# Kernel tuning notes

Hardware: AMD Instinct MI355X
Metric: run time of the kernel (lower is better)

The kernel has to match this reference:

```python
import jax, jax.numpy as jnp
import numpy as np

N = 50000   # number of cells/nodes
C = 256     # in_channels
H = 4       # num_heads
D = 64      # out_channels (per-head)
E = 800000  # number of edges (avg degree 16)


def setup_inputs() -> dict:
    key = jax.random.key(0)
    ks = jax.random.split(key, 10)
    s = 1.0 / np.sqrt(C)  # torch nn.Linear default init bound
    u = lambda k, shape: jax.random.uniform(k, shape, jnp.float32, -s, s)
    return {
        "query_input": jax.random.normal(ks[0], (N, C), jnp.float32),
        "source_input": jax.random.normal(ks[1], (N, C), jnp.float32),
        "Wq_w": u(ks[2], (H * D, C)), "Wq_b": u(ks[3], (H * D,)),
        "Wk_w": u(ks[4], (H * D, C)), "Wk_b": u(ks[5], (H * D,)),
        "Wv_w": u(ks[6], (H * D, C)), "Wv_b": u(ks[7], (H * D,)),
        "edge_index": jax.random.randint(ks[8], (2, E), 0, N),
        "edge_weight": jax.random.uniform(ks[9], (E,), jnp.float32),
    }


def reference(query_input, source_input, Wq_w, Wq_b, Wk_w, Wk_b, Wv_w, Wv_b,
              edge_index, edge_weight):
    n = query_input.shape[0]
    q = (query_input @ Wq_w.T + Wq_b).reshape(n, H, D)
    k = (source_input @ Wk_w.T + Wk_b).reshape(n, H, D)
    v = (source_input @ Wv_w.T + Wv_b).reshape(n, H, D)

    # --- linear (kernelized) attention, global Frobenius normalization ---
    qs = q / jnp.linalg.norm(q)
    ksn = k / jnp.linalg.norm(k)
    kvs = jnp.einsum('lhm,lhd->hmd', ksn, v)               # [H,M,D]
    attn_num = jnp.einsum('nhm,hmd->nhd', qs, kvs)
    attn_num = attn_num + v.sum(axis=0)[None]              # + vs_sum broadcast
    ks_sum = ksn.sum(axis=0)                               # [H,M]
    normalizer = jnp.einsum('nhm,hm->nh', qs, ks_sum)[..., None] + jnp.float32(n)
    attn_out = attn_num / normalizer                       # [N,H,D]

    # --- GCN aggregation on value: out[col] += w * d_norm_in * d_norm_out * v[row] ---
    row, col = edge_index[0], edge_index[1]
    d = jnp.zeros((n,), jnp.float32).at[col].add(1.0)      # in-degree on col
    d_norm_in = jnp.sqrt(1.0 / d[col])
    d_norm_out = jnp.sqrt(1.0 / d[row])
    val = jnp.nan_to_num(edge_weight * d_norm_in * d_norm_out,
                         nan=0.0, posinf=0.0, neginf=0.0)  # [E]
    gathered = v[row] * val[:, None, None]                 # [E,H,D]
    gcn_out = jax.ops.segment_sum(gathered, col, num_segments=n)  # [N,H,D]

    return (attn_out + gcn_out).mean(axis=1)               # [N,D]
```

## Files before the change

kernel.cpp:

```cpp
#include <hip/hip_runtime.h>
#include <hip/hip_bf16.h>

#define N_NODES 50000
#define N_EDGES 800000
#define NBUK 512
#define BWID 98
#define BCAP 2048
#define PCHUNK 1024
#define PBLK 782
#define NVS 32

typedef __bf16 bf16x8 __attribute__((ext_vector_type(8)));
typedef float f32x4 __attribute__((ext_vector_type(4)));

__device__ __forceinline__ unsigned short f2bf(float f) {
    unsigned int u = __builtin_bit_cast(unsigned int, f);
    u += 0x7fffu + ((u >> 16) & 1u);
    return (unsigned short)(u >> 16);
}
__device__ __forceinline__ float bf2f(unsigned short s) {
    return __uint_as_float((unsigned int)s << 16);
}

__device__ __forceinline__ void gld_lds16(const void* g, void* lds) {
    __builtin_amdgcn_global_load_lds(
        (const __attribute__((address_space(1))) unsigned int*)g,
        (__attribute__((address_space(3))) unsigned int*)lds, 16, 0, 0);
}

__global__ __launch_bounds__(256) void k_wprep(const float* __restrict__ Wv,
                                               const float* __restrict__ bv,
                                               unsigned short* __restrict__ wvbar,
                                               float* __restrict__ bvbar) {
    int idx = blockIdx.x * 256 + threadIdx.x;
    int d = idx >> 6;
    int c0 = (idx & 63) * 4;
    const float4* W4 = (const float4*)Wv;
    float4 w0 = W4[((d) * 256 + c0) >> 2];
    float4 w1 = W4[((64 + d) * 256 + c0) >> 2];
    float4 w2 = W4[((128 + d) * 256 + c0) >> 2];
    float4 w3 = W4[((192 + d) * 256 + c0) >> 2];
    ushort4 s;
    s.x = f2bf(0.25f * (w0.x + w1.x + w2.x + w3.x));
    s.y = f2bf(0.25f * (w0.y + w1.y + w2.y + w3.y));
    s.z = f2bf(0.25f * (w0.z + w1.z + w2.z + w3.z));
    s.w = f2bf(0.25f * (w0.w + w1.w + w2.w + w3.w));
    int ks = c0 >> 5;
    int q  = (c0 >> 3) & 3;
    int j0 = c0 & 7;
    int nf = d >> 4;
    int ln = d & 15;
    int base = ((ks * 4 + nf) * 64 + q * 16 + ln) * 8 + j0;
    *(ushort4*)&wvbar[base] = s;
    if (blockIdx.x == 0 && threadIdx.x < 64) {
        int t = threadIdx.x;
        bvbar[t] = 0.25f * (bv[t] + bv[64 + t] + bv[128 + t] + bv[192 + t]);
    }
}

__global__ __launch_bounds__(256) void k_part(const int* __restrict__ ei,
                                              const float* __restrict__ ew,
                                              int* __restrict__ gcur,
                                              uint2* __restrict__ bkt)
{
    __shared__ int hist[NBUK];
    __shared__ int cur[NBUK];
    const int t = threadIdx.x;
    const int e0 = blockIdx.x * PCHUNK;
    hist[t] = 0; hist[t + 256] = 0;
    __syncthreads();
    #pragma unroll
    for (int k = 0; k < PCHUNK / 256; ++k) {
        int e = e0 + k * 256 + t;
        if (e < N_EDGES) {
            int c = ei[N_EDGES + e];
            atomicAdd(&hist[c / BWID], 1);
        }
    }
    __syncthreads();
    {
        int b = t;
        if (hist[b]) cur[b] = b * BCAP + atomicAdd(&gcur[b], hist[b]);
        b = t + 256;
        if (hist[b]) cur[b] = b * BCAP + atomicAdd(&gcur[b], hist[b]);
    }
    __syncthreads();
    #pragma unroll
    for (int k = 0; k < PCHUNK / 256; ++k) {
        int e = e0 + k * 256 + t;
        if (e < N_EDGES) {
            int c = ei[N_EDGES + e];
            int b = c / BWID;
            int row = ei[e];
            float w = ew[e];
            int slot = atomicAdd(&cur[b], 1);
            if (slot < (b + 1) * BCAP) {
                uint2 en;
                en.x = ((unsigned int)row << 16) | (unsigned int)f2bf(w);
                en.y = (unsigned int)(c - b * BWID);
                bkt[slot] = en;
            }
        }
    }
}

__global__ __launch_bounds__(256) void k_bucket(const int* __restrict__ gcur,
                                                const uint2* __restrict__ bkt,
                                                int* __restrict__ deg,
                                                int* __restrict__ off,
                                                unsigned int* __restrict__ srt)
{
    __shared__ int hist[128];
    __shared__ int lcur[128];
    const int t = threadIdx.x;
    const int b = blockIdx.x;
    if (t < 128) hist[t] = 0;
    __syncthreads();
    const int cnt = min(gcur[b], BCAP);
    const uint2* base = bkt + (size_t)b * BCAP;
    for (int i = t; i < cnt; i += 256)
        atomicAdd(&hist[base[i].y], 1);
    __syncthreads();
    const int v = (t < 128) ? hist[t] : 0;
    #pragma unroll
    for (int d = 1; d < 128; d <<= 1) {
        int u = (t >= d && t < 128) ? hist[t - d] : 0;
        __syncthreads();
        if (t >= d && t < 128) hist[t] += u;
        __syncthreads();
    }
    if (t < 128) {
        int excl = hist[t] - v;
        lcur[t] = excl;
        if (t < BWID) {
            int col = b * BWID + t;
            if (col < N_NODES) {
                deg[col] = v;
                off[col] = b * BCAP + excl;
            }
        }
    }
    __syncthreads();
    unsigned int* sb = srt + (size_t)b * BCAP;
    for (int i = t; i < cnt; i += 256) {
        uint2 en = base[i];
        int pos = atomicAdd(&lcur[en.y], 1);
        sb[pos] = en.x;
    }
}

__global__ __launch_bounds__(256) void k_vbar(
    const float* __restrict__ Xs, const unsigned short* __restrict__ wvbar,
    const float* __restrict__ bvbar, const int* __restrict__ deg,
    unsigned short* __restrict__ vbarh, float* __restrict__ vsumr)
{
    __shared__ float lX[64 * 128];
    const int t = threadIdx.x;
    const int w = t >> 6;
    const int l = t & 63;
    const int ln = l & 15;
    const int q = l >> 4;
    const int n0 = blockIdx.x * 64;

    const char* Xc = (const char*)Xs;
    const bf16x8* Wf = (const bf16x8*)wvbar;
    const unsigned int swzl = ((unsigned int)(ln & 7)) << 4;
    const char* lrow = (const char*)&lX[(w * 16 + ln) * 128];

    f32x4 acc[4];
    #pragma unroll
    for (int nf = 0; nf < 4; ++nf) acc[nf] = (f32x4){0.f, 0.f, 0.f, 0.f};

    #pragma unroll
    for (int h = 0; h < 2; ++h) {
        #pragma unroll
        for (int i = 0; i < 8; ++i) {
            int r = w * 16 + i * 2 + (l >> 5);
            int g = n0 + r;
            int gc = (g < N_NODES) ? g : 0;
            unsigned int off = ((unsigned int)((l & 31) * 16))
                             ^ (((unsigned int)(r & 7)) << 4);
            const void* src = Xc + (size_t)gc * 1024 + (unsigned int)(h * 512) + off;
            gld_lds16(src, &lX[(w * 16 + i * 2) * 128]);
        }
        asm volatile("s_waitcnt vmcnt(0)" ::: "memory");
        __builtin_amdgcn_sched_barrier(0);

        #pragma unroll
        for (int ks2 = 0; ks2 < 4; ++ks2) {
            unsigned int c0 = (unsigned int)(ks2 * 128 + q * 32);
            float4 xa = *(const float4*)(lrow + (c0 ^ swzl));
            float4 xb = *(const float4*)(lrow + ((c0 + 16u) ^ swzl));
            bf16x8 A;
            A[0] = (__bf16)xa.x; A[1] = (__bf16)xa.y;
            A[2] = (__bf16)xa.z; A[3] = (__bf16)xa.w;
            A[4] = (__bf16)xb.x; A[5] = (__bf16)xb.y;
            A[6] = (__bf16)xb.z; A[7] = (__bf16)xb.w;
            int ks = h * 4 + ks2;
            #pragma unroll
            for (int nf = 0; nf < 4; ++nf) {
                bf16x8 b = Wf[(ks * 4 + nf) * 64 + l];
                acc[nf] = __builtin_amdgcn_mfma_f32_16x16x32_bf16(A, b, acc[nf], 0, 0, 0);
            }
        }
        if (h == 0) {
            asm volatile("s_waitcnt lgkmcnt(0)" ::: "memory");
            __builtin_amdgcn_sched_barrier(0);
        }
    }

    float bvb[4];
    #pragma unroll
    for (int nf = 0; nf < 4; ++nf) bvb[nf] = bvbar[nf * 16 + ln];
    float psum[4] = {0.f, 0.f, 0.f, 0.f};
    #pragma unroll
    for (int r4 = 0; r4 < 4; ++r4) {
        int g = n0 + w * 16 + q * 4 + r4;
        bool ok = g < N_NODES;
        float sc = 0.f;
        if (ok) {
            float dg = (float)deg[g];
            sc = (dg > 0.f) ? __frsqrt_rn(dg) : 0.f;
        }
        #pragma unroll
        for (int nf = 0; nf < 4; ++nf) {
            if (ok) {
                vbarh[g * 64 + nf * 16 + ln] = f2bf((acc[nf][r4] + bvb[nf]) * sc);
                psum[nf] += acc[nf][r4];
            }
        }
    }
    #pragma unroll
    for (int nf = 0; nf < 4; ++nf) {
        float v = psum[nf];
        v += __shfl_xor(v, 16, 64);
        v += __shfl_xor(v, 32, 64);
        psum[nf] = v;
    }
    if (l < 16) {
        int rep = (blockIdx.x * 4 + w) & (NVS - 1);
        #pragma unroll
        for (int nf = 0; nf < 4; ++nf)
            atomicAdd(&vsumr[rep * 64 + nf * 16 + ln], psum[nf]);
    }
}

__global__ __launch_bounds__(256) void k_gather(
    const int* __restrict__ off, const int* __restrict__ deg,
    const unsigned int* __restrict__ srt, const unsigned short* __restrict__ vbarh,
    const float* __restrict__ vsumr, const float* __restrict__ bvbar,
    float* __restrict__ out)
{
    const int t = threadIdx.x;
    const int lane = t & 63;
    const int n = blockIdx.x * 4 + (t >> 6);
    if (n >= N_NODES) return;
    const int e0 = off[n];
    const int dc = deg[n];
    const int e1 = e0 + dc;
    float acc = 0.f;
    int e = e0;
    for (; e + 3 < e1; e += 4) {
        unsigned int p0 = srt[e];
        unsigned int p1 = srt[e + 1];
        unsigned int p2 = srt[e + 2];
        unsigned int p3 = srt[e + 3];
        float a0 = __uint_as_float(p0 << 16) * bf2f(vbarh[(p0 >> 16) * 64 + lane]);
        float a1 = __uint_as_float(p1 << 16) * bf2f(vbarh[(p1 >> 16) * 64 + lane]);
        float a2 = __uint_as_float(p2 << 16) * bf2f(vbarh[(p2 >> 16) * 64 + lane]);
        float a3 = __uint_as_float(p3 << 16) * bf2f(vbarh[(p3 >> 16) * 64 + lane]);
        acc += (a0 + a1) + (a2 + a3);
    }
    for (; e < e1; ++e) {
        unsigned int p = srt[e];
        acc += __uint_as_float(p << 16) * bf2f(vbarh[(p >> 16) * 64 + lane]);
    }
    float dcf = (float)dc;
    float scn = (dcf > 0.f) ? __frsqrt_rn(dcf) : 0.f;
    float vs = 0.f;
    #pragma unroll
    for (int i = 0; i < NVS; ++i) vs += vsumr[i * 64 + lane];
    float aconst = vs * (1.0f / (float)N_NODES) + bvbar[lane];
    out[n * 64 + lane] = acc * scn + aconst;
}

extern "C" void kernel_launch(void* const* d_in, const int* in_sizes, int n_in,
                              void* d_out, int out_size, void* d_ws, size_t ws_size,
                              hipStream_t stream)
{
    const float* Xs = (const float*)d_in[1];
    const float* Wv = (const float*)d_in[6];
    const float* bv = (const float*)d_in[7];
    const int*   ei = (const int*)d_in[8];
    const float* ew = (const float*)d_in[9];
    float* out = (float*)d_out;

    unsigned short* vbarh = (unsigned short*)d_ws;
    uint2* bkt  = (uint2*)(vbarh + (size_t)N_NODES * 64);
    unsigned int* srt = (unsigned int*)(bkt + (size_t)NBUK * BCAP);
    unsigned short* wvbar = (unsigned short*)(srt + (size_t)NBUK * BCAP);
    float* bvbar   = (float*)(wvbar + 16384);
    float* vsumr   = bvbar + 64;
    int*   gcur    = (int*)(vsumr + NVS * 64);
    int*   deg     = gcur + NBUK;
    int*   off     = deg + N_NODES;

    hipMemsetAsync(vsumr, 0, (size_t)(NVS * 64 + NBUK) * 4, stream);
    k_wprep<<<16, 256, 0, stream>>>(Wv, bv, wvbar, bvbar);
    k_part<<<PBLK, 256, 0, stream>>>(ei, ew, gcur, bkt);
    k_bucket<<<NBUK, 256, 0, stream>>>(gcur, bkt, deg, off, srt);
    k_vbar<<<(N_NODES + 63) / 64, 256, 0, stream>>>(Xs, wvbar, bvbar, deg, vbarh, vsumr);
    k_gather<<<(NBUK * BWID) / 4, 256, 0, stream>>>(off, deg, srt, vbarh, vsumr, bvbar, out);
}
```

Before: 215.2 us.

## Stage edge partition and bucket sort through LDS for coalesced global writes

The partition kernel now processes larger chunks per block, does a local prefix sum over bucket counts, and sorts entries by bucket in shared memory before writing them out, so global stores to each bucket become contiguous runs instead of scattered single writes. The bucket-sort kernel likewise scatters into an LDS staging buffer and then writes the sorted bucket back with coalesced stores. Together these aim to cut the cost of random global writes in the CSR build, at the price of more shared memory, extra barriers and a serial scan, plus fewer partition blocks.

After: 210.5 us. 2.2% less time.

```diff
diff --git a/kernel.cpp b/kernel.cpp
--- a/kernel.cpp
+++ b/kernel.cpp
@@ -6,8 +6,8 @@
 #define NBUK 512
 #define BWID 98
 #define BCAP 2048
-#define PCHUNK 1024
-#define PBLK 782
+#define PCHUNK 4096
+#define PBLK 196
 #define NVS 32
 
 typedef __bf16 bf16x8 __attribute__((ext_vector_type(8)));
@@ -64,25 +64,45 @@
                                               uint2* __restrict__ bkt)
 {
     __shared__ int hist[NBUK];
-    __shared__ int cur[NBUK];
+    __shared__ int s2[256];
+    __shared__ int lstart[NBUK];
+    __shared__ int lcur[NBUK];
+    __shared__ int gbase[NBUK];
+    __shared__ uint2 lent[PCHUNK];
+    __shared__ unsigned int ldst[PCHUNK];
     const int t = threadIdx.x;
     const int e0 = blockIdx.x * PCHUNK;
+    const int cnt = min(N_EDGES - e0, PCHUNK);
+
     hist[t] = 0; hist[t + 256] = 0;
     __syncthreads();
     #pragma unroll
     for (int k = 0; k < PCHUNK / 256; ++k) {
         int e = e0 + k * 256 + t;
-        if (e < N_EDGES) {
-            int c = ei[N_EDGES + e];
-            atomicAdd(&hist[c / BWID], 1);
-        }
+        if (e < N_EDGES) atomicAdd(&hist[ei[N_EDGES + e] / BWID], 1);
     }
     __syncthreads();
     {
         int b = t;
-        if (hist[b]) cur[b] = b * BCAP + atomicAdd(&gcur[b], hist[b]);
+        if (hist[b]) gbase[b] = b * BCAP + atomicAdd(&gcur[b], hist[b]);
         b = t + 256;
-        if (hist[b]) cur[b] = b * BCAP + atomicAdd(&gcur[b], hist[b]);
+        if (hist[b]) gbase[b] = b * BCAP + atomicAdd(&gcur[b], hist[b]);
+    }
+    s2[t] = hist[2 * t] + hist[2 * t + 1];
+    __syncthreads();
+    #pragma unroll
+    for (int d = 1; d < 256; d <<= 1) {
+        int u = (t >= d) ? s2[t - d] : 0;
+        __syncthreads();
+        s2[t] += u;
+        __syncthreads();
+    }
+    {
+        int b0 = (t > 0) ? s2[t - 1] : 0;
+        lstart[2 * t] = b0;
+        lstart[2 * t + 1] = b0 + hist[2 * t];
+        lcur[2 * t] = b0;
+        lcur[2 * t + 1] = b0 + hist[2 * t];
     }
     __syncthreads();
     #pragma unroll
@@ -91,16 +111,19 @@
         if (e < N_EDGES) {
             int c = ei[N_EDGES + e];
             int b = c / BWID;
-            int row = ei[e];
-            float w = ew[e];
-            int slot = atomicAdd(&cur[b], 1);
-            if (slot < (b + 1) * BCAP) {
-                uint2 en;
-                en.x = ((unsigned int)row << 16) | (unsigned int)f2bf(w);
-                en.y = (unsigned int)(c - b * BWID);
-                bkt[slot] = en;
-            }
-        }
+            int lp = atomicAdd(&lcur[b], 1);
+            uint2 en;
+            en.x = ((unsigned int)ei[e] << 16) | (unsigned int)f2bf(ew[e]);
+            en.y = (unsigned int)(c - b * BWID);
+            lent[lp] = en;
+            unsigned int gd = (unsigned int)(gbase[b] + (lp - lstart[b]));
+            ldst[lp] = (gd < (unsigned int)((b + 1) * BCAP)) ? gd : 0xFFFFFFFFu;
+        }
+    }
+    __syncthreads();
+    for (int j = t; j < cnt; j += 256) {
+        unsigned int gd = ldst[j];
+        if (gd != 0xFFFFFFFFu) bkt[gd] = lent[j];
     }
 }
 
@@ -112,6 +135,7 @@
 {
     __shared__ int hist[128];
     __shared__ int lcur[128];
+    __shared__ unsigned int stg[BCAP];
     const int t = threadIdx.x;
     const int b = blockIdx.x;
     if (t < 128) hist[t] = 0;
@@ -141,12 +165,14 @@
         }
     }
     __syncthreads();
-    unsigned int* sb = srt + (size_t)b * BCAP;
     for (int i = t; i < cnt; i += 256) {
         uint2 en = base[i];
         int pos = atomicAdd(&lcur[en.y], 1);
-        sb[pos] = en.x;
-    }
+        stg[pos] = en.x;
+    }
+    __syncthreads();
+    unsigned int* sb = srt + (size_t)b * BCAP;
+    for (int i = t; i < cnt; i += 256) sb[i] = stg[i];
 }
 
 __global__ __launch_bounds__(256) void k_vbar(
```
